# Kernel optimization log

Measured on AMD Instinct MI355X. Metric: run time of the kernel, lower is better.

Reference implementation:

```python
import jax, jax.numpy as jnp
import numpy as np

B, D, C, L, H, HF, HG, NCLS = 4096, 2048, 16, 128, 256, 512, 128, 200

def _init(key, shape, fan_in):
    return jax.random.normal(key, shape, dtype=jnp.float32) * (1.0 / np.sqrt(fan_in))

def setup_inputs() -> dict:
    key = jax.random.key(0)
    ks = jax.random.split(key, 16)
    return {
        "x": jax.random.normal(ks[0], (B, D), dtype=jnp.float32),
        "fp": jax.random.uniform(ks[1], (C, D), minval=-1.0, maxval=1.0, dtype=jnp.float32),  # probability_vector_logits
        "mean_inputs": jax.random.normal(ks[2], (D,), dtype=jnp.float32) * 0.1,
        "Wg1": _init(ks[3], (C, D, H), D), "bg1": jnp.zeros((C, H), jnp.float32),
        "Wg2": _init(ks[4], (C, H, L), H), "bg2": jnp.zeros((C, L), jnp.float32),
        "Wf1": _init(ks[5], (D, HF), D), "bf1": jnp.zeros((HF,), jnp.float32),
        "Wf2": _init(ks[6], (HF, L), HF), "bf2": jnp.zeros((L,), jnp.float32),
        "Wg_head": _init(ks[7], (C * (L // 2), HG), C * (L // 2)), "bg_head": jnp.zeros((HG,), jnp.float32),
        "Wc": _init(ks[8], (HG, NCLS), HG), "bc": jnp.zeros((NCLS,), jnp.float32),
    }

def _l2_normalize(v, axis):
    # tf.math.l2_normalize: v * rsqrt(max(sum(v^2), 1e-12))
    sq = jnp.sum(v * v, axis=axis, keepdims=True)
    return v * jax.lax.rsqrt(jnp.maximum(sq, 1e-12))

def reference(x, fp, mean_inputs, Wg1, bg1, Wg2, bg2, Wf1, bf1, Wf2, bf2, Wg_head, bg_head, Wc, bc):
    # Deterministic forward (training=False, forward_deterministic=True)
    gate = jax.nn.sigmoid(fp)  # [C, D]
    # mask_features: gate*x + (1-gate)*mean, vectorized over concepts -> [C, B, D]
    masked = gate[:, None, :] * x[None, :, :] + (1.0 - gate)[:, None, :] * mean_inputs[None, None, :]
    # per-concept generator MLPs (distinct weights per concept) -> concept_matrix [B, C, L]
    h = jax.nn.relu(jnp.einsum('cbd,cdh->cbh', masked, Wg1) + bg1[:, None, :])
    cm = jnp.einsum('cbh,chl->cbl', h, Wg2) + bg2[:, None, :]
    cm = jnp.transpose(cm, (1, 0, 2))              # [B, C, L]
    cm_norm = _l2_normalize(cm, axis=1)            # normalize across concept axis (axis=1 in TF code)
    # shared features_to_concepts model applied to each masked_x -> latent [C, B, L]
    hf = jax.nn.relu(jnp.einsum('cbd,dh->cbh', masked, Wf1) + bf1)
    latent = jnp.einsum('cbh,hl->cbl', hf, Wf2) + bf2
    latent = jnp.transpose(latent, (1, 0, 2))      # [B, C, L]
    # concept scores: sigmoid(<cm_norm[b,c,:], latent[b,c,:]>)
    concept_prob = jax.nn.sigmoid(jnp.sum(cm_norm * latent, axis=-1))  # [B, C]
    half = L // 2
    p = concept_prob[:, :, None]
    bottleneck = p * cm_norm[:, :, half:] + (1.0 - p) * cm_norm[:, :, :half]  # [B, C, L/2]
    bottleneck = bottleneck.reshape(bottleneck.shape[0], -1)                   # [B, C*L/2]
    # g_model + concepts_to_labels head
    z = jax.nn.relu(bottleneck @ Wg_head + bg_head)
    logits = z @ Wc + bc  # [B, NCLS]
    return logits
```

## Files before the change

### kernel.cpp

```cpp
#include <hip/hip_runtime.h>
#include <hip/hip_bf16.h>

typedef __bf16 bf16;
typedef __attribute__((ext_vector_type(8))) __bf16 bf16x8;
typedef __attribute__((ext_vector_type(4))) float f32x4;

__device__ __forceinline__ void gload_lds16(const void* g, void* l) {
    __builtin_amdgcn_global_load_lds(
        (const __attribute__((address_space(1))) unsigned int*)g,
        (__attribute__((address_space(3))) unsigned int*)l, 16, 0, 0);
}

#define BARRIER()   asm volatile("s_barrier" ::: "memory")
#define WAITLGKM0() asm volatile("s_waitcnt lgkmcnt(0)" ::: "memory")
#define WAITVM4()   asm volatile("s_waitcnt vmcnt(4)" ::: "memory")
#define WAITVM0()   asm volatile("s_waitcnt vmcnt(0)" ::: "memory")
#define SCHED0()    __builtin_amdgcn_sched_barrier(0)

__device__ __forceinline__ unsigned int pack2(float a, float b) {
    bf16 x = (bf16)a, y = (bf16)b;
    unsigned short ux, uy;
    __builtin_memcpy(&ux, &x, 2); __builtin_memcpy(&uy, &y, 2);
    return (unsigned int)ux | ((unsigned int)uy << 16);
}

__global__ void prep_all(const float* __restrict__ x, bf16* __restrict__ xbf,
                         const float* __restrict__ fp, const float* __restrict__ mean,
                         const float* __restrict__ Wg1, const float* __restrict__ Wf1,
                         bf16* __restrict__ Wall,
                         float* __restrict__ corr_g, float* __restrict__ corr_f,
                         const float* __restrict__ Wg2, bf16* __restrict__ Wg2T,
                         const float* __restrict__ Wf2, bf16* __restrict__ Wf2T,
                         const float* __restrict__ Wgh, bf16* __restrict__ WghT)
{
    __shared__ float tile[32][33];
    const int b = blockIdx.x;
    const int t = threadIdx.x;

    if (b < 192) {
        const int isF = (b >= 64);
        const int bb  = isF ? b - 64 : b;
        const int nsb = isF ? 8 : 4;
        const int c   = bb / nsb;
        const int sblk = bb % nsb;
        const int S   = isF ? 512 : 256;
        const float* W = isF ? Wf1 : (Wg1 + (long)c * 2048 * 256);
        float* corr = isF ? corr_f : corr_g;
        const int sl = t & 63;
        const int s  = sblk * 64 + sl;
        const int w  = t >> 6;
        const float* fpc = fp + c * 2048;
        float acc = 0.f;
#pragma unroll 4
        for (int r = w; r < 2048; r += 4) {
            const float g = 1.f / (1.f + expf(-fpc[r]));
            acc = fmaf((1.f - g) * mean[r], W[(long)r * S + s], acc);
        }
        float* red = &tile[0][0];
        red[w * 64 + sl] = acc;
        __syncthreads();
        if (w == 0)
            corr[(long)c * S + s] = red[sl] + red[64 + sl] + red[128 + sl] + red[192 + sl];
        return;
    }
    if (b < 2240) {
        const int i = b - 192;
        const int s0 = (i & 15) * 32;
        const int r0 = ((i >> 4) & 63) * 32;
        const int zz = i >> 10;
        const int tx = t & 31, ty = t >> 5;
#pragma unroll
        for (int k = 0; k < 32; k += 8)
            tile[ty + k][tx] = Wf1[(long)(r0 + ty + k) * 512 + s0 + tx];
        __syncthreads();
#pragma unroll 1
        for (int j = 0; j < 8; ++j) {
            const int z = zz * 8 + j;
            bf16* out = Wall + (long)z * 768 * 2048 + (long)256 * 2048;
            const float gv = 1.f / (1.f + expf(-fp[z * 2048 + r0 + tx]));
#pragma unroll
            for (int k = 0; k < 32; k += 8)
                out[(long)(s0 + ty + k) * 2048 + r0 + tx] = (bf16)(gv * tile[tx][ty + k]);
        }
        return;
    }
    if (b < 10432) {
        const int i = b - 2240;
        const int s0 = (i & 7) * 32;
        const int r0 = ((i >> 3) & 63) * 32;
        const int z  = i >> 9;
        const int tx = t & 31, ty = t >> 5;
        const float* in = Wg1 + (long)z * 2048 * 256;
        bf16* out = Wall + (long)z * 768 * 2048;
#pragma unroll
        for (int k = 0; k < 32; k += 8)
            tile[ty + k][tx] = in[(long)(r0 + ty + k) * 256 + s0 + tx];
        __syncthreads();
        const float gv = 1.f / (1.f + expf(-fp[z * 2048 + r0 + tx]));
#pragma unroll
        for (int k = 0; k < 32; k += 8)
            out[(long)(s0 + ty + k) * 2048 + r0 + tx] = (bf16)(gv * tile[tx][ty + k]);
        return;
    }
    if (b < 14528) {
        const long i = ((long)(b - 10432) * 256 + t) * 8;
        float4 v0 = *(const float4*)(x + i);
        float4 v1 = *(const float4*)(x + i + 4);
        bf16x8 o;
        o[0]=(bf16)v0.x; o[1]=(bf16)v0.y; o[2]=(bf16)v0.z; o[3]=(bf16)v0.w;
        o[4]=(bf16)v1.x; o[5]=(bf16)v1.y; o[6]=(bf16)v1.z; o[7]=(bf16)v1.w;
        *(bf16x8*)(xbf + i) = o;
        return;
    }
    {
        const int i = b - 14528;
        const float* in; bf16* out; int R, bx, by;
        if (i < 512) {
            const int z = i >> 5, rem = i & 31;
            bx = rem & 3; by = rem >> 2; R = 256;
            in = Wg2 + (long)z * 256 * 128; out = Wg2T + (long)z * 128 * 256;
        } else if (i < 576) {
            const int rem = i - 512;
            bx = rem & 3; by = rem >> 2; R = 512;
            in = Wf2; out = Wf2T;
        } else {
            const int rem = i - 576;
            bx = rem & 3; by = rem >> 2; R = 1024;
            in = Wgh; out = WghT;
        }
        const int s0 = bx * 32, r0 = by * 32;
        const int tx = t & 31, ty = t >> 5;
#pragma unroll
        for (int k = 0; k < 32; k += 8)
            tile[ty + k][tx] = in[(long)(r0 + ty + k) * 128 + s0 + tx];
        __syncthreads();
#pragma unroll
        for (int k = 0; k < 32; k += 8)
            out[(long)(s0 + ty + k) * R + r0 + tx] = (bf16)tile[tx][ty + k];
    }
}

__global__ __launch_bounds__(512, 2)
void gemm256(const bf16* __restrict__ A, const bf16* __restrict__ Wall,
             const float* __restrict__ bg1, const float* __restrict__ corr_g,
             const float* __restrict__ bf1, const float* __restrict__ corr_f,
             bf16* __restrict__ h_out, bf16* __restrict__ hf_out)
{
    __shared__ __align__(16) bf16 lds[2][4][8192];

    const int bid = blockIdx.x;
    const int swz = (bid & 7) * 96 + (bid >> 3);
    const int c   = swz / 48;
    const int rem = swz % 48;
    const int ny  = rem / 16;
    const int m0  = (rem % 16) * 256;

    const int t = threadIdx.x, lane = t & 63, w = t >> 6;
    const int wr = w >> 2, wc = w & 3;
    const bf16* Bc = Wall + (long)c * 768 * 2048;

    const int rr = lane >> 3;
    const int qq = (lane & 7) ^ rr;
    const bf16* pA0 = A  + (long)(m0 + w * 16 + rr) * 2048 + qq * 8;
    const bf16* pA1 = pA0 + 8 * 2048;
    const bf16* pB0 = Bc + (long)(ny * 256 + w * 16 + rr) * 2048 + qq * 8;
    const bf16* pB1 = pB0 + 8 * 2048;

    const int l15 = lane & 15;
    const int q0 = (((lane >> 4) ^ (lane & 7))) * 8;
    const int aoff0 = l15 * 64 + q0, aoff1 = aoff0 ^ 32;
    const int boff0 = ((wc & 1) * 64 + l15) * 64 + q0, boff1 = boff0 ^ 32;
    const int hb = 2 + (wc >> 1);

    f32x4 acc[8][4] = {};
    bf16x8 Ax[4][2], Ay[4][2], Bx[2][2], By[2][2];

#define STG(buf, half, P0, P1, e) do { \
    gload_lds16((P0) + (e), &lds[buf][half][w * 1024]); \
    gload_lds16((P1) + (e), &lds[buf][half][w * 1024 + 512]); } while (0)

#define RDA(dst, buf, mb) do { _Pragma("unroll") \
    for (int mm = 0; mm < 4; ++mm) { \
        dst[mm][0] = *(const bf16x8*)&lds[buf][wr][aoff0 + (mb + mm) * 1024]; \
        dst[mm][1] = *(const bf16x8*)&lds[buf][wr][aoff1 + (mb + mm) * 1024]; } } while (0)

#define RDB(dst, buf, nh) do { _Pragma("unroll") \
    for (int nn = 0; nn < 2; ++nn) { \
        dst[nn][0] = *(const bf16x8*)&lds[buf][hb][boff0 + (nh * 2 + nn) * 1024]; \
        dst[nn][1] = *(const bf16x8*)&lds[buf][hb][boff1 + (nh * 2 + nn) * 1024]; } } while (0)

#define MFMA16(mb, Af, Bf, nh) do { __builtin_amdgcn_s_setprio(1); _Pragma("unroll") \
    for (int kk = 0; kk < 2; ++kk) { _Pragma("unroll") \
      for (int mm = 0; mm < 4; ++mm) { _Pragma("unroll") \
        for (int nn = 0; nn < 2; ++nn) { \
            acc[mb + mm][nh * 2 + nn] = __builtin_amdgcn_mfma_f32_16x16x32_bf16( \
                Af[mm][kk], Bf[nn][kk], acc[mb + mm][nh * 2 + nn], 0, 0, 0); } } } \
    __builtin_amdgcn_s_setprio(0); } while (0)

    STG(0, 0, pA0, pA1, 0);
    STG(0, 1, pA0, pA1, 262144);
    STG(0, 2, pB0, pB1, 0);
    STG(0, 3, pB0, pB1, 262144);
    STG(1, 2, pB0, pB1, 64);
    STG(1, 3, pB0, pB1, 262144 + 64);
    WAITVM4();
    BARRIER();
    RDA(Ax, 0, 0); RDB(Bx, 0, 0);

#pragma unroll 1
    for (int it = 0; it < 15; ++it) {
        const int kB  = (2 * it + 1) * 64;
        const int kA2 = (2 * it + 2) * 64;
        const int kB2 = (2 * it + 3) * 64;
        STG(1, 0, pA0, pA1, kB);
        BARRIER();
        RDB(By, 0, 1);
        SCHED0();
        MFMA16(0, Ax, Bx, 0);
        BARRIER();
        STG(1, 1, pA0, pA1, 262144 + kB);
        BARRIER();
        RDA(Ay, 0, 4);
        SCHED0();
        MFMA16(0, Ax, By, 1);
        BARRIER();
        STG(0, 2, pB0, pB1, kA2);
        BARRIER();
        MFMA16(4, Ay, By, 1);
        BARRIER();
        STG(0, 3, pB0, pB1, 262144 + kA2);
        WAITVM4();
        BARRIER();
        RDA(Ax, 1, 0);
        SCHED0();
        MFMA16(4, Ay, Bx, 0);
        RDB(Bx, 1, 0);
        BARRIER();
        STG(0, 0, pA0, pA1, kA2);
        BARRIER();
        RDB(By, 1, 1);
        SCHED0();
        MFMA16(0, Ax, Bx, 0);
        BARRIER();
        STG(0, 1, pA0, pA1, 262144 + kA2);
        BARRIER();
        RDA(Ay, 1, 4);
        SCHED0();
        MFMA16(0, Ax, By, 1);
        BARRIER();
        STG(1, 2, pB0, pB1, kB2);
        BARRIER();
        MFMA16(4, Ay, By, 1);
        BARRIER();
        STG(1, 3, pB0, pB1, 262144 + kB2);
        WAITVM4();
        BARRIER();
        RDA(Ax, 0, 0);
        SCHED0();
        MFMA16(4, Ay, Bx, 0);
        RDB(Bx, 0, 0);
        BARRIER();
    }

    {
        const int kB = 31 * 64;
        STG(1, 0, pA0, pA1, kB);
        BARRIER();
        RDB(By, 0, 1);
        SCHED0();
        MFMA16(0, Ax, Bx, 0);
        BARRIER();
        STG(1, 1, pA0, pA1, 262144 + kB);
        BARRIER();
        RDA(Ay, 0, 4);
        SCHED0();
        MFMA16(0, Ax, By, 1);
        BARRIER();
        MFMA16(4, Ay, By, 1);
        BARRIER();
        WAITVM0();
        BARRIER();
        RDA(Ax, 1, 0);
        SCHED0();
        MFMA16(4, Ay, Bx, 0);
        RDB(Bx, 1, 0);
        BARRIER();
        RDB(By, 1, 1);
        SCHED0();
        MFMA16(0, Ax, Bx, 0);
        BARRIER();
        RDA(Ay, 1, 4);
        SCHED0();
        MFMA16(0, Ax, By, 1);
        BARRIER();
        MFMA16(4, Ay, By, 1);
        MFMA16(4, Ay, Bx, 0);
    }

    WAITLGKM0();
    BARRIER();
    bf16* cst = (bf16*)&lds[0][0][0];
    const int r4 = (lane >> 4) * 4;
    const int isH = (ny == 0);
    const int N = isH ? 256 : 512;
#pragma unroll
    for (int n = 0; n < 4; ++n) {
        const int cl = wc * 64 + n * 16 + l15;
        float bv;
        if (isH) bv = bg1[c * 256 + cl] + corr_g[c * 256 + cl];
        else {
            const int cf = (ny - 1) * 256 + cl;
            bv = bf1[cf] + corr_f[c * 512 + cf];
        }
#pragma unroll
        for (int m = 0; m < 8; ++m)
#pragma unroll
            for (int j = 0; j < 4; ++j) {
                const int row = wr * 128 + m * 16 + r4 + j;
                cst[row * 256 + cl] = (bf16)fmaxf(acc[m][n][j] + bv, 0.0f);
            }
    }
    BARRIER();
    bf16* obase = isH ? h_out + ((long)c * 4096 + m0) * 256
                      : hf_out + ((long)c * 4096 + m0) * 512 + (ny - 1) * 256;
    const int trow = t >> 5, tch = (t & 31) * 8;
#pragma unroll
    for (int pass = 0; pass < 16; ++pass) {
        const int row = pass * 16 + trow;
        *(bf16x8*)&obase[(long)row * N + tch] = *(const bf16x8*)&cst[row * 256 + tch];
    }
#undef STG
#undef RDA
#undef RDB
#undef MFMA16
}

__global__ __launch_bounds__(256, 2)
void gemm_mid(const bf16* __restrict__ h, const bf16* __restrict__ hf,
              const bf16* __restrict__ Wg2T, const bf16* __restrict__ Wf2T,
              const float* __restrict__ bg2, const float* __restrict__ bf2,
              bf16* __restrict__ cm, bf16* __restrict__ lat)
{
    __shared__ __align__(16) bf16 As[128 * 64];
    __shared__ __align__(16) bf16 Bs[128 * 64];

    const int z  = blockIdx.z;
    const int m0 = blockIdx.x * 128;
    const int t  = threadIdx.x;
    const int lane = t & 63, wave = t >> 6;
    const int wr = wave >> 1, wc = wave & 1;

    int K; const bf16 *Ac, *W; const float* bias; bf16* outp;
    if (z < 16) {
        K = 256; Ac = h + (long)z * 4096 * 256; W = Wg2T + (long)z * 128 * 256;
        bias = bg2 + z * 128; outp = cm + (long)m0 * 2048 + z * 128;
    } else {
        const int c = z - 16;
        K = 512; Ac = hf + (long)c * 4096 * 512; W = Wf2T;
        bias = bf2; outp = lat + (long)m0 * 2048 + c * 128;
    }

    const int sr = t >> 3;
    const int sc = (t & 7) * 8;

    f32x4 acc[4][4] = {};

    for (int kt = 0; kt < K / 64; ++kt) {
        const int k0 = kt * 64;
#pragma unroll
        for (int i = 0; i < 4; ++i)
            gload_lds16(Ac + (long)(m0 + i * 32 + sr) * K + k0 + sc, &As[i * 2048 + wave * 512]);
#pragma unroll
        for (int i = 0; i < 4; ++i)
            gload_lds16(W + (long)(i * 32 + sr) * K + k0 + sc, &Bs[i * 2048 + wave * 512]);
        __syncthreads();

#pragma unroll
        for (int kk = 0; kk < 2; ++kk) {
            bf16x8 af[4], bfr[4];
#pragma unroll
            for (int m = 0; m < 4; ++m)
                af[m] = *(const bf16x8*)&As[(wr * 64 + m * 16 + (lane & 15)) * 64 + kk * 32 + (lane >> 4) * 8];
#pragma unroll
            for (int n = 0; n < 4; ++n)
                bfr[n] = *(const bf16x8*)&Bs[(wc * 64 + n * 16 + (lane & 15)) * 64 + kk * 32 + (lane >> 4) * 8];
#pragma unroll
            for (int m = 0; m < 4; ++m)
#pragma unroll
                for (int n = 0; n < 4; ++n)
                    acc[m][n] = __builtin_amdgcn_mfma_f32_16x16x32_bf16(af[m], bfr[n], acc[m][n], 0, 0, 0);
        }
        __syncthreads();
    }

    const int ci = lane & 15, r4 = (lane >> 4) * 4;
#pragma unroll
    for (int m = 0; m < 4; ++m)
#pragma unroll
        for (int n = 0; n < 4; ++n) {
            const int col = wc * 64 + n * 16 + ci;
            const float bv = bias[col];
#pragma unroll
            for (int j = 0; j < 4; ++j) {
                const int row = wr * 64 + m * 16 + r4 + j;
                outp[(long)row * 2048 + col] = (bf16)(acc[m][n][j] + bv);
            }
        }
}

__global__ __launch_bounds__(256, 2)
void gemm_zp(const bf16* __restrict__ A, const bf16* __restrict__ Wt,
             bf16* __restrict__ outb)
{
    __shared__ __align__(16) bf16 As[128 * 64];
    __shared__ __align__(16) bf16 Bs[128 * 64];

    const int z  = blockIdx.z;
    const int m0 = blockIdx.x * 128;
    const int t  = threadIdx.x;
    const int lane = t & 63, wave = t >> 6;
    const int wr = wave >> 1, wc = wave & 1;

    const bf16* Ac = A  + (long)z * 128;
    const bf16* W  = Wt + (long)z * 128;
    bf16* outp = outb + (long)z * 4096 * 128 + (long)m0 * 128;

    const int sr = t >> 3;
    const int sc = (t & 7) * 8;

    f32x4 acc[4][4] = {};

    for (int kt = 0; kt < 2; ++kt) {
        const int k0 = kt * 64;
#pragma unroll
        for (int i = 0; i < 4; ++i)
            gload_lds16(Ac + (long)(m0 + i * 32 + sr) * 1024 + k0 + sc, &As[i * 2048 + wave * 512]);
#pragma unroll
        for (int i = 0; i < 4; ++i)
            gload_lds16(W + (long)(i * 32 + sr) * 1024 + k0 + sc, &Bs[i * 2048 + wave * 512]);
        __syncthreads();

#pragma unroll
        for (int kk = 0; kk < 2; ++kk) {
            bf16x8 af[4], bfr[4];
#pragma unroll
            for (int m = 0; m < 4; ++m)
                af[m] = *(const bf16x8*)&As[(wr * 64 + m * 16 + (lane & 15)) * 64 + kk * 32 + (lane >> 4) * 8];
#pragma unroll
            for (int n = 0; n < 4; ++n)
                bfr[n] = *(const bf16x8*)&Bs[(wc * 64 + n * 16 + (lane & 15)) * 64 + kk * 32 + (lane >> 4) * 8];
#pragma unroll
            for (int m = 0; m < 4; ++m)
#pragma unroll
                for (int n = 0; n < 4; ++n)
                    acc[m][n] = __builtin_amdgcn_mfma_f32_16x16x32_bf16(af[m], bfr[n], acc[m][n], 0, 0, 0);
        }
        __syncthreads();
    }

    const int ci = lane & 15, r4 = (lane >> 4) * 4;
#pragma unroll
    for (int m = 0; m < 4; ++m)
#pragma unroll
        for (int n = 0; n < 4; ++n) {
            const int col = wc * 64 + n * 16 + ci;
#pragma unroll
            for (int j = 0; j < 4; ++j) {
                const int row = wr * 64 + m * 16 + r4 + j;
                outp[(long)row * 128 + col] = (bf16)acc[m][n][j];
            }
        }
}

__global__ void fuse_kernel(const unsigned int* __restrict__ cm, const unsigned int* __restrict__ lat,
                            unsigned int* __restrict__ bott)
{
    const int wave = threadIdx.x >> 6;
    const int l    = threadIdx.x & 63;
    const int b    = blockIdx.x * 4 + wave;
    const unsigned int* cu = cm  + (size_t)b * 1024;
    const unsigned int* lu = lat + (size_t)b * 1024;

    float c0[16], c1[16], l0[16], l1[16];
    float sq0 = 0.f, sq1 = 0.f;
#pragma unroll
    for (int c = 0; c < 16; ++c) {
        const unsigned int vc = cu[c * 64 + l], vl = lu[c * 64 + l];
        c0[c] = __uint_as_float(vc << 16);
        c1[c] = __uint_as_float(vc & 0xffff0000u);
        l0[c] = __uint_as_float(vl << 16);
        l1[c] = __uint_as_float(vl & 0xffff0000u);
        sq0 += c0[c] * c0[c]; sq1 += c1[c] * c1[c];
    }
    const float rs0 = rsqrtf(fmaxf(sq0, 1e-12f));
    const float rs1 = rsqrtf(fmaxf(sq1, 1e-12f));
#pragma unroll
    for (int c = 0; c < 16; ++c) {
        const float cn0 = c0[c] * rs0, cn1 = c1[c] * rs1;
        float part = cn0 * l0[c] + cn1 * l1[c];
#pragma unroll
        for (int off = 32; off; off >>= 1) part += __shfl_xor(part, off);
        const float p = 1.0f / (1.0f + expf(-part));
        const float o0 = __shfl_xor(cn0, 32), o1 = __shfl_xor(cn1, 32);
        if (l < 32)
            bott[(size_t)b * 512 + c * 32 + l] =
                pack2(p * o0 + (1.f - p) * cn0, p * o1 + (1.f - p) * cn1);
    }
}

__global__ void head2_kernel(const bf16* __restrict__ zp, const float* __restrict__ bgh,
                             const float* __restrict__ Wc, const float* __restrict__ bc,
                             float* __restrict__ out)
{
    __shared__ float zs[8][128];
    const int b0 = blockIdx.x * 8;
    const int t = threadIdx.x;
#pragma unroll
    for (int i = 0; i < 4; ++i) {
        const int idx = t + i * 256;
        const int r = idx >> 7, k = idx & 127;
        float s = bgh[k];
#pragma unroll
        for (int ks = 0; ks < 8; ++ks)
            s += (float)zp[(size_t)ks * 524288 + (size_t)(b0 + r) * 128 + k];
        zs[r][k] = fmaxf(s, 0.0f);
    }
    __syncthreads();
    if (t < 200) {
        float a[8];
#pragma unroll
        for (int r = 0; r < 8; ++r) a[r] = bc[t];
        for (int k = 0; k < 128; ++k) {
            const float wv = Wc[k * 200 + t];
#pragma unroll
            for (int r = 0; r < 8; ++r) a[r] = fmaf(zs[r][k], wv, a[r]);
        }
#pragma unroll
        for (int r = 0; r < 8; ++r) out[(size_t)(b0 + r) * 200 + t] = a[r];
    }
}


extern "C" void kernel_launch(void* const* d_in, const int* in_sizes, int n_in,
                              void* d_out, int out_size, void* d_ws, size_t ws_size,
                              hipStream_t stream)
{
    (void)in_sizes; (void)n_in; (void)out_size; (void)ws_size;

    const float* x    = (const float*)d_in[0];
    const float* fp   = (const float*)d_in[1];
    const float* mean = (const float*)d_in[2];
    const float* Wg1  = (const float*)d_in[3];
    const float* bg1  = (const float*)d_in[4];
    const float* Wg2  = (const float*)d_in[5];
    const float* bg2  = (const float*)d_in[6];
    const float* Wf1  = (const float*)d_in[7];
    const float* bf1  = (const float*)d_in[8];
    const float* Wf2  = (const float*)d_in[9];
    const float* bf2  = (const float*)d_in[10];
    const float* Wgh  = (const float*)d_in[11];
    const float* bgh  = (const float*)d_in[12];
    const float* Wc   = (const float*)d_in[13];
    const float* bc   = (const float*)d_in[14];
    float* outp = (float*)d_out;

    char* p = (char*)d_ws;
    size_t off = 0;
    auto alloc = [&](size_t bytes) { void* r = p + off; off += (bytes + 255) & ~(size_t)255; return r; };
    bf16*  xbf    = (bf16*) alloc((size_t)4096 * 2048 * 2);
    bf16*  Wall   = (bf16*) alloc((size_t)16 * 768 * 2048 * 2);
    bf16*  Wg2T   = (bf16*) alloc((size_t)16 * 128 * 256 * 2);
    bf16*  Wf2T   = (bf16*) alloc((size_t)128 * 512 * 2);
    bf16*  WghT   = (bf16*) alloc((size_t)128 * 1024 * 2);
    float* corr_g = (float*)alloc((size_t)16 * 256 * 4);
    float* corr_f = (float*)alloc((size_t)16 * 512 * 4);
    bf16*  h      = (bf16*) alloc((size_t)16 * 4096 * 256 * 2);
    bf16*  hf     = (bf16*) alloc((size_t)16 * 4096 * 512 * 2);
    bf16*  cm     = (bf16*) alloc((size_t)4096 * 2048 * 2);
    bf16*  lat    = (bf16*) alloc((size_t)4096 * 2048 * 2);
    bf16*  bott   = (bf16*) alloc((size_t)4096 * 1024 * 2);
    bf16*  zp     = (bf16*) alloc((size_t)8 * 4096 * 128 * 2);

    prep_all<<<15232, 256, 0, stream>>>(x, xbf, fp, mean, Wg1, Wf1, Wall,
                                        corr_g, corr_f, Wg2, Wg2T, Wf2, Wf2T, Wgh, WghT);

    gemm256<<<768, 512, 0, stream>>>(xbf, Wall, bg1, corr_g, bf1, corr_f, h, hf);

    gemm_mid<<<dim3(32, 1, 32), 256, 0, stream>>>(h, hf, Wg2T, Wf2T, bg2, bf2, cm, lat);

    fuse_kernel<<<1024, 256, 0, stream>>>((const unsigned int*)cm, (const unsigned int*)lat,
                                          (unsigned int*)bott);

    gemm_zp<<<dim3(32, 1, 8), 256, 0, stream>>>(bott, WghT, zp);

    head2_kernel<<<512, 256, 0, stream>>>(zp, bgh, Wc, bc, outp);
}
```

Baseline: 307.5 us.

## Fuse Wg2 second-layer GEMM into gemm256 epilogue for generator branch

For the generator branch (ny==0), the relu'd hidden tile is kept in LDS and multiplied by Wg2T right inside gemm256, which then writes cm directly. The 16x4096x256 h intermediate is no longer written or read back, and the cm half of gemm_mid goes away, leaving a smaller gemm_lat kernel for the latent path. The LDS staging tile is now XOR-swizzled to cut bank conflicts on the new fragment reads. In exchange, the ny==0 blocks do extra epilogue work with B fragments loaded straight from global memory, so those blocks run longer than the others.

```diff
diff --git a/kernel.cpp b/kernel.cpp
--- a/kernel.cpp
+++ b/kernel.cpp
@@ -144,7 +144,8 @@
 void gemm256(const bf16* __restrict__ A, const bf16* __restrict__ Wall,
              const float* __restrict__ bg1, const float* __restrict__ corr_g,
              const float* __restrict__ bf1, const float* __restrict__ corr_f,
-             bf16* __restrict__ h_out, bf16* __restrict__ hf_out)
+             const bf16* __restrict__ Wg2T, const float* __restrict__ bg2,
+             bf16* __restrict__ cm_out, bf16* __restrict__ hf_out)
 {
     __shared__ __align__(16) bf16 lds[2][4][8192];
 
@@ -302,7 +303,6 @@
     bf16* cst = (bf16*)&lds[0][0][0];
     const int r4 = (lane >> 4) * 4;
     const int isH = (ny == 0);
-    const int N = isH ? 256 : 512;
 #pragma unroll
     for (int n = 0; n < 4; ++n) {
         const int cl = wc * 64 + n * 16 + l15;
@@ -317,17 +317,55 @@
 #pragma unroll
             for (int j = 0; j < 4; ++j) {
                 const int row = wr * 128 + m * 16 + r4 + j;
-                cst[row * 256 + cl] = (bf16)fmaxf(acc[m][n][j] + bv, 0.0f);
+                cst[row * 256 + (cl ^ ((row & 7) << 4))] = (bf16)fmaxf(acc[m][n][j] + bv, 0.0f);
             }
     }
     BARRIER();
-    bf16* obase = isH ? h_out + ((long)c * 4096 + m0) * 256
-                      : hf_out + ((long)c * 4096 + m0) * 512 + (ny - 1) * 256;
-    const int trow = t >> 5, tch = (t & 31) * 8;
-#pragma unroll
-    for (int pass = 0; pass < 16; ++pass) {
-        const int row = pass * 16 + trow;
-        *(bf16x8*)&obase[(long)row * N + tch] = *(const bf16x8*)&cst[row * 256 + tch];
+    if (isH) {
+        const bf16* Wp = Wg2T + (long)c * 128 * 256;
+        f32x4 a2[2][8] = {};
+        const int rb = w * 32;
+#pragma unroll 1
+        for (int ks = 0; ks < 8; ++ks) {
+            bf16x8 af2[2], bqr[8];
+            const int k0 = ks * 32 + (lane >> 4) * 8;
+#pragma unroll
+            for (int mt = 0; mt < 2; ++mt) {
+                const int row = rb + mt * 16 + l15;
+                af2[mt] = *(const bf16x8*)&cst[row * 256 + (k0 ^ ((row & 7) << 4))];
+            }
+#pragma unroll
+            for (int nt = 0; nt < 8; ++nt)
+                bqr[nt] = *(const bf16x8*)&Wp[(long)(nt * 16 + l15) * 256 + k0];
+#pragma unroll
+            for (int mt = 0; mt < 2; ++mt)
+#pragma unroll
+                for (int nt = 0; nt < 8; ++nt)
+                    a2[mt][nt] = __builtin_amdgcn_mfma_f32_16x16x32_bf16(
+                        af2[mt], bqr[nt], a2[mt][nt], 0, 0, 0);
+        }
+        bf16* cmp = cm_out + (long)(m0 + rb) * 2048 + c * 128;
+#pragma unroll
+        for (int mt = 0; mt < 2; ++mt)
+#pragma unroll
+            for (int nt = 0; nt < 8; ++nt) {
+                const int col = nt * 16 + l15;
+                const float bv2 = bg2[c * 128 + col];
+#pragma unroll
+                for (int j = 0; j < 4; ++j) {
+                    const int row = mt * 16 + r4 + j;
+                    cmp[(long)row * 2048 + col] = (bf16)(a2[mt][nt][j] + bv2);
+                }
+            }
+    } else {
+        bf16* obase = hf_out + ((long)c * 4096 + m0) * 512 + (ny - 1) * 256;
+        const int trow = t >> 5, tch = (t & 31) * 8;
+#pragma unroll
+        for (int pass = 0; pass < 16; ++pass) {
+            const int row = pass * 16 + trow;
+            *(bf16x8*)&obase[(long)row * 512 + tch] =
+                *(const bf16x8*)&cst[row * 256 + (tch ^ ((row & 7) << 4))];
+        }
     }
 #undef STG
 #undef RDA
@@ -336,43 +374,34 @@
 }
 
 __global__ __launch_bounds__(256, 2)
-void gemm_mid(const bf16* __restrict__ h, const bf16* __restrict__ hf,
-              const bf16* __restrict__ Wg2T, const bf16* __restrict__ Wf2T,
-              const float* __restrict__ bg2, const float* __restrict__ bf2,
-              bf16* __restrict__ cm, bf16* __restrict__ lat)
+void gemm_lat(const bf16* __restrict__ hf, const bf16* __restrict__ Wf2T,
+              const float* __restrict__ bf2, bf16* __restrict__ lat)
 {
     __shared__ __align__(16) bf16 As[128 * 64];
     __shared__ __align__(16) bf16 Bs[128 * 64];
 
-    const int z  = blockIdx.z;
+    const int cidx = blockIdx.z;
     const int m0 = blockIdx.x * 128;
     const int t  = threadIdx.x;
     const int lane = t & 63, wave = t >> 6;
     const int wr = wave >> 1, wc = wave & 1;
 
-    int K; const bf16 *Ac, *W; const float* bias; bf16* outp;
-    if (z < 16) {
-        K = 256; Ac = h + (long)z * 4096 * 256; W = Wg2T + (long)z * 128 * 256;
-        bias = bg2 + z * 128; outp = cm + (long)m0 * 2048 + z * 128;
-    } else {
-        const int c = z - 16;
-        K = 512; Ac = hf + (long)c * 4096 * 512; W = Wf2T;
-        bias = bf2; outp = lat + (long)m0 * 2048 + c * 128;
-    }
+    const bf16* Ac = hf + (long)cidx * 4096 * 512;
+    bf16* outp = lat + (long)m0 * 2048 + cidx * 128;
 
     const int sr = t >> 3;
     const int sc = (t & 7) * 8;
 
     f32x4 acc[4][4] = {};
 
-    for (int kt = 0; kt < K / 64; ++kt) {
+    for (int kt = 0; kt < 8; ++kt) {
         const int k0 = kt * 64;
 #pragma unroll
         for (int i = 0; i < 4; ++i)
-            gload_lds16(Ac + (long)(m0 + i * 32 + sr) * K + k0 + sc, &As[i * 2048 + wave * 512]);
+            gload_lds16(Ac + (long)(m0 + i * 32 + sr) * 512 + k0 + sc, &As[i * 2048 + wave * 512]);
 #pragma unroll
         for (int i = 0; i < 4; ++i)
-            gload_lds16(W + (long)(i * 32 + sr) * K + k0 + sc, &Bs[i * 2048 + wave * 512]);
+            gload_lds16(Wf2T + (long)(i * 32 + sr) * 512 + k0 + sc, &Bs[i * 2048 + wave * 512]);
         __syncthreads();
 
 #pragma unroll
@@ -399,7 +428,7 @@
 #pragma unroll
         for (int n = 0; n < 4; ++n) {
             const int col = wc * 64 + n * 16 + ci;
-            const float bv = bias[col];
+            const float bv = bf2[col];
 #pragma unroll
             for (int j = 0; j < 4; ++j) {
                 const int row = wr * 64 + m * 16 + r4 + j;
@@ -574,7 +603,6 @@
     bf16*  WghT   = (bf16*) alloc((size_t)128 * 1024 * 2);
     float* corr_g = (float*)alloc((size_t)16 * 256 * 4);
     float* corr_f = (float*)alloc((size_t)16 * 512 * 4);
-    bf16*  h      = (bf16*) alloc((size_t)16 * 4096 * 256 * 2);
     bf16*  hf     = (bf16*) alloc((size_t)16 * 4096 * 512 * 2);
     bf16*  cm     = (bf16*) alloc((size_t)4096 * 2048 * 2);
     bf16*  lat    = (bf16*) alloc((size_t)4096 * 2048 * 2);
@@ -584,9 +612,10 @@
     prep_all<<<15232, 256, 0, stream>>>(x, xbf, fp, mean, Wg1, Wf1, Wall,
                                         corr_g, corr_f, Wg2, Wg2T, Wf2, Wf2T, Wgh, WghT);
 
-    gemm256<<<768, 512, 0, stream>>>(xbf, Wall, bg1, corr_g, bf1, corr_f, h, hf);
-
-    gemm_mid<<<dim3(32, 1, 32), 256, 0, stream>>>(h, hf, Wg2T, Wf2T, bg2, bf2, cm, lat);
+    gemm256<<<768, 512, 0, stream>>>(xbf, Wall, bg1, corr_g, bf1, corr_f,
+                                     Wg2T, bg2, cm, hf);
+
+    gemm_lat<<<dim3(32, 1, 16), 256, 0, stream>>>(hf, Wf2T, bf2, lat);
 
     fuse_kernel<<<1024, 256, 0, stream>>>((const unsigned int*)cm, (const unsigned int*)lat,
                                           (unsigned int*)bott);
```

Measured after the change: 312.3 us. No clear change (+1.6%).
